# Kernel tuning notes

Hardware: AMD Instinct MI355X
Metric: run time of the kernel (lower is better)

The kernel has to match this reference:

```python
import jax, jax.numpy as jnp
import numpy as np

N_EXPERTS = 6
TOP_K = 2
AUX_COEFF = 0.01
W_SCALE = 0.02  # keep activations in a sane range with random weights


def setup_inputs() -> dict:
    key = jax.random.key(0)
    k1, k2, k3, k4 = jax.random.split(key, 4)
    B, T, D, H = 4, 2048, 1024, 4096
    x = jax.random.normal(k1, (B, T, D), dtype=jnp.float32)
    w_router = jax.random.normal(k2, (D, N_EXPERTS), dtype=jnp.float32) * W_SCALE
    w1 = jax.random.normal(k3, (N_EXPERTS, D, H), dtype=jnp.float32) * W_SCALE
    w2 = jax.random.normal(k4, (N_EXPERTS, H, D), dtype=jnp.float32) * W_SCALE
    return {"x": x, "w_router": w_router, "w1": w1, "w2": w2}


def reference(x, w_router, w1, w2):
    B, T, D = x.shape
    x_flat = x.reshape(-1, D)                              # (N, D)
    router_logits = x_flat @ w_router                      # (N, E)
    router_probs = jax.nn.softmax(router_logits, axis=-1)
    top_probs, top_idx = jax.lax.top_k(router_probs, TOP_K)  # (N, K)
    top_probs = top_probs / jnp.sum(top_probs, axis=-1, keepdims=True)
    # combine weights per (token, expert): sum over k slots hitting expert e
    onehot = jax.nn.one_hot(top_idx, N_EXPERTS, dtype=x.dtype)  # (N, K, E)
    comb = jnp.einsum('nke,nk->ne', onehot, top_probs)          # (N, E)
    out = jnp.zeros_like(x_flat)
    for e in range(N_EXPERTS):
        h = jax.nn.gelu(x_flat @ w1[e], approximate=False)      # (N, H)
        out = out + comb[:, e:e + 1] * (h @ w2[e])              # (N, D)
    tokens_per_expert = jnp.mean(router_probs, axis=0)          # (E,)
    uniform = jnp.full_like(tokens_per_expert, 1.0 / N_EXPERTS)
    aux_loss = AUX_COEFF * jnp.mean((tokens_per_expert - uniform) ** 2)
    return out.reshape(B, T, D), aux_loss
```

## Files before the change

### kernel.cpp

```cpp
#include <hip/hip_runtime.h>

#define N_TOK 8192
#define DDIM  1024
#define HDIM  4096
#define NEXP  6
#define RBLOCKS (N_TOK / 4)
#define SBLOCKS 32

typedef unsigned short ushort_t;
typedef __bf16 bf16_t;
typedef bf16_t bf16x8 __attribute__((ext_vector_type(8)));
typedef float f32x4 __attribute__((ext_vector_type(4)));

typedef const __attribute__((address_space(1))) void* gptr_t;
typedef __attribute__((address_space(3))) void* lptr_t;

__device__ __forceinline__ void g2l16(const void* g, void* l) {
    __builtin_amdgcn_global_load_lds((gptr_t)g, (lptr_t)l, 16, 0, 0);
}

__device__ __forceinline__ ushort_t f2bf(float f) {
    unsigned int u = __float_as_uint(f);
    unsigned int r = (u + 0x7FFFu + ((u >> 16) & 1u)) >> 16;
    return (ushort_t)r;
}

__global__ void transpose_bf16_kernel(const float* __restrict__ src, ushort_t* __restrict__ dst,
                                      int R, int C) {
    __shared__ float tile[32][33];
    size_t msz = (size_t)R * C;
    src += (size_t)blockIdx.z * msz;
    dst += (size_t)blockIdx.z * msz;
    int c0 = blockIdx.x * 32, r0 = blockIdx.y * 32;
    int tx = threadIdx.x & 31, ty = threadIdx.x >> 5;
#pragma unroll
    for (int i = 0; i < 4; ++i)
        tile[ty + 8 * i][tx] = src[(size_t)(r0 + ty + 8 * i) * C + c0 + tx];
    __syncthreads();
#pragma unroll
    for (int i = 0; i < 4; ++i)
        dst[(size_t)(c0 + ty + 8 * i) * R + r0 + tx] = f2bf(tile[tx][ty + 8 * i]);
}

__global__ void router_kernel(const float* __restrict__ x, const float* __restrict__ wr,
                              ushort_t* __restrict__ xb,
                              int* __restrict__ tok_e, float* __restrict__ tok_w,
                              float* __restrict__ part_p, int* __restrict__ part_c) {
    __shared__ float bsum[NEXP];
    __shared__ int bcnt[NEXP];
    int wid = threadIdx.x >> 6, l = threadIdx.x & 63;
    if (threadIdx.x < NEXP) { bsum[threadIdx.x] = 0.f; bcnt[threadIdx.x] = 0; }
    __syncthreads();
    int t = blockIdx.x * 4 + wid;
    const float* xr = x + (size_t)t * DDIM;
    ushort_t* xbr = xb + (size_t)t * DDIM;
    float acc[NEXP] = {0.f, 0.f, 0.f, 0.f, 0.f, 0.f};
#pragma unroll
    for (int c = 0; c < 4; ++c) {
        int k0 = c * 256 + l * 4;
        float4 xv = *(const float4*)(xr + k0);
        union { ushort_t u[4]; uint2 v; } ob;
        ob.u[0] = f2bf(xv.x); ob.u[1] = f2bf(xv.y); ob.u[2] = f2bf(xv.z); ob.u[3] = f2bf(xv.w);
        *(uint2*)(xbr + k0) = ob.v;
        float wv[24];
#pragma unroll
        for (int q = 0; q < 6; ++q)
            *(float4*)(wv + 4 * q) = *(const float4*)(wr + (size_t)k0 * NEXP + 4 * q);
        float xa[4] = {xv.x, xv.y, xv.z, xv.w};
#pragma unroll
        for (int r = 0; r < 4; ++r)
#pragma unroll
            for (int e = 0; e < NEXP; ++e) acc[e] += xa[r] * wv[r * NEXP + e];
    }
#pragma unroll
    for (int e = 0; e < NEXP; ++e)
#pragma unroll
        for (int d = 32; d >= 1; d >>= 1) acc[e] += __shfl_xor(acc[e], d);
    if (l == 0) {
        float m = acc[0];
#pragma unroll
        for (int e = 1; e < NEXP; ++e) m = fmaxf(m, acc[e]);
        float p[NEXP], s = 0.f;
#pragma unroll
        for (int e = 0; e < NEXP; ++e) { p[e] = expf(acc[e] - m); s += p[e]; }
        float inv = 1.0f / s;
#pragma unroll
        for (int e = 0; e < NEXP; ++e) p[e] *= inv;
        int i1 = 0; float b1 = p[0];
#pragma unroll
        for (int e = 1; e < NEXP; ++e) if (p[e] > b1) { b1 = p[e]; i1 = e; }
        int i2 = -1; float b2 = -1.f;
#pragma unroll
        for (int e = 0; e < NEXP; ++e) if (e != i1 && p[e] > b2) { b2 = p[e]; i2 = e; }
        float swn = 1.0f / (b1 + b2);
        tok_e[2 * t] = i1; tok_e[2 * t + 1] = i2;
        tok_w[2 * t] = b1 * swn; tok_w[2 * t + 1] = b2 * swn;
        atomicAdd(&bcnt[i1], 1);
        atomicAdd(&bcnt[i2], 1);
#pragma unroll
        for (int e = 0; e < NEXP; ++e) atomicAdd(&bsum[e], p[e]);
    }
    __syncthreads();
    if (threadIdx.x < NEXP) {
        part_p[(size_t)blockIdx.x * NEXP + threadIdx.x] = bsum[threadIdx.x];
        part_c[(size_t)blockIdx.x * NEXP + threadIdx.x] = bcnt[threadIdx.x];
    }
}

__global__ void finalize_kernel(const float* __restrict__ part_p, const int* __restrict__ part_c,
                                int* __restrict__ counts, int* __restrict__ offs,
                                float* __restrict__ aux_out) {
    __shared__ float redp[NEXP][4];
    __shared__ int redc[NEXP][4];
    int tid = threadIdx.x, wid = tid >> 6, l = tid & 63;
    float myp[NEXP] = {0.f, 0.f, 0.f, 0.f, 0.f, 0.f};
    int myc[NEXP] = {0, 0, 0, 0, 0, 0};
    for (int b = tid; b < RBLOCKS; b += 256) {
#pragma unroll
        for (int e = 0; e < NEXP; ++e) {
            myp[e] += part_p[(size_t)b * NEXP + e];
            myc[e] += part_c[(size_t)b * NEXP + e];
        }
    }
#pragma unroll
    for (int e = 0; e < NEXP; ++e) {
#pragma unroll
        for (int d = 32; d >= 1; d >>= 1) {
            myp[e] += __shfl_xor(myp[e], d);
            myc[e] += __shfl_xor(myc[e], d);
        }
        if (l == 0) { redp[e][wid] = myp[e]; redc[e][wid] = myc[e]; }
    }
    __syncthreads();
    if (tid == 0) {
        int o = 0;
        float s = 0.f;
        for (int e = 0; e < NEXP; ++e) {
            int c = redc[e][0] + redc[e][1] + redc[e][2] + redc[e][3];
            float ps = redp[e][0] + redp[e][1] + redp[e][2] + redp[e][3];
            counts[e] = c;
            offs[e] = o;
            o += c;
            float d = ps / (float)N_TOK - (1.0f / 6.0f);
            s += d * d;
        }
        offs[NEXP] = o;
        aux_out[0] = 0.01f * (s / 6.0f);
    }
}

__global__ void scatter_kernel(const int* __restrict__ tok_e, const float* __restrict__ tok_w,
                               const int* __restrict__ offs, int* __restrict__ cursors,
                               int* __restrict__ slot_token, float* __restrict__ slot_w) {
    __shared__ int lcnt[NEXP], lbase[NEXP];
    int tid = threadIdx.x;
    if (tid < NEXP) lcnt[tid] = 0;
    __syncthreads();
    int t = blockIdx.x * 256 + tid;
    int e0 = tok_e[2 * t], e1 = tok_e[2 * t + 1];
    int r0 = atomicAdd(&lcnt[e0], 1);
    int r1 = atomicAdd(&lcnt[e1], 1);
    __syncthreads();
    if (tid < NEXP) lbase[tid] = atomicAdd(&cursors[tid], lcnt[tid]);
    __syncthreads();
    int i0 = offs[e0] + lbase[e0] + r0;
    slot_token[i0] = t; slot_w[i0] = tok_w[2 * t];
    int i1 = offs[e1] + lbase[e1] + r1;
    slot_token[i1] = t; slot_w[i1] = tok_w[2 * t + 1];
}

template <int LAYER>
__global__ __launch_bounds__(256, 2)
void moe_gemm_kernel(const ushort_t* __restrict__ A, const ushort_t* __restrict__ Bt,
                     ushort_t* __restrict__ Hout, float* __restrict__ Out,
                     const int* __restrict__ slot_token, const float* __restrict__ slot_w,
                     const int* __restrict__ offs, const int* __restrict__ counts) {
    constexpr int Kd = (LAYER == 1) ? DDIM : HDIM;
    constexpr int Nd = (LAYER == 1) ? HDIM : DDIM;
    const int e = blockIdx.z;
    const int cnt = counts[e];
    const int mbase = blockIdx.y * 128;
    if (mbase >= cnt) return;
    const int nbase = blockIdx.x * 256;
    const int off = offs[e];
    const ushort_t* Bte = Bt + (size_t)e * ((size_t)Nd * Kd);

    __shared__ __align__(16) ushort_t sA[128 * 32];
    __shared__ __align__(16) ushort_t sB[256 * 32];

    const int tid = threadIdx.x;
    const int wid = tid >> 6, l = tid & 63;

    size_t aoff[2];
#pragma unroll
    for (int j = 0; j < 2; ++j) {
        int p = j * 256 + tid;
        int row = p >> 2, slot = p & 3;
        int cs = slot ^ ((row >> 1) & 3);
        int gr = mbase + row;
        int grc = gr < cnt - 1 ? gr : cnt - 1;
        size_t arow = (LAYER == 1) ? (size_t)slot_token[off + grc] * DDIM
                                   : (size_t)(off + grc) * HDIM;
        aoff[j] = arow + (size_t)cs * 8;
    }
    size_t boff[4];
#pragma unroll
    for (int j = 0; j < 4; ++j) {
        int p = j * 256 + tid;
        int row = p >> 2, slot = p & 3;
        int cs = slot ^ ((row >> 1) & 3);
        boff[j] = (size_t)(nbase + row) * Kd + (size_t)cs * 8;
    }

    const int lm = l & 15, kg = l >> 4;
    const int wm = (wid & 1) * 64, wn = (wid >> 1) * 128;
    const char* sAb = (const char*)sA;
    const char* sBb = (const char*)sB;
    int aOffs[4], bOffs[8];
#pragma unroll
    for (int fr = 0; fr < 4; ++fr) {
        int ar = wm + fr * 16 + lm;
        aOffs[fr] = ar * 64 + ((kg ^ ((ar >> 1) & 3)) << 4);
    }
#pragma unroll
    for (int fr = 0; fr < 8; ++fr) {
        int br = wn + fr * 16 + lm;
        bOffs[fr] = br * 64 + ((kg ^ ((br >> 1) & 3)) << 4);
    }

    f32x4 acc[4][8] = {};

    for (int kt = 0; kt < Kd; kt += 32) {
        g2l16(A + aoff[0] + kt,   sA + wid * 512);
        g2l16(A + aoff[1] + kt,   sA + 2048 + wid * 512);
        g2l16(Bte + boff[0] + kt, sB + wid * 512);
        g2l16(Bte + boff[1] + kt, sB + 2048 + wid * 512);
        g2l16(Bte + boff[2] + kt, sB + 4096 + wid * 512);
        g2l16(Bte + boff[3] + kt, sB + 6144 + wid * 512);
        __syncthreads();
        bf16x8 af[4], bfv[8];
#pragma unroll
        for (int fr = 0; fr < 4; ++fr) af[fr] = *(const bf16x8*)(sAb + aOffs[fr]);
#pragma unroll
        for (int fr = 0; fr < 8; ++fr) bfv[fr] = *(const bf16x8*)(sBb + bOffs[fr]);
#pragma unroll
        for (int i = 0; i < 4; ++i)
#pragma unroll
            for (int n = 0; n < 8; ++n)
                acc[i][n] = __builtin_amdgcn_mfma_f32_16x16x32_bf16(af[i], bfv[n], acc[i][n], 0, 0, 0);
        __syncthreads();
    }

    if (LAYER == 1) {
#pragma unroll
        for (int i = 0; i < 4; ++i) {
#pragma unroll
            for (int r = 0; r < 4; ++r) {
                int grow = mbase + wm + i * 16 + kg * 4 + r;
                if (grow < cnt) {
                    size_t hbase = (size_t)(off + grow) * HDIM + nbase + wn + lm;
#pragma unroll
                    for (int n = 0; n < 8; ++n) {
                        float v = acc[i][n][r];
                        float u = -1.5957691216f * v * (1.0f + 0.044715f * v * v);
                        float g = v / (1.0f + __expf(u));
                        Hout[hbase + n * 16] = f2bf(g);
                    }
                }
            }
        }
    } else {
#pragma unroll
        for (int i = 0; i < 4; ++i) {
#pragma unroll
            for (int r = 0; r < 4; ++r) {
                int grow = mbase + wm + i * 16 + kg * 4 + r;
                if (grow < cnt) {
                    int si = off + grow;
                    int tok = slot_token[si];
                    float wgt = slot_w[si];
                    float* obase = Out + (size_t)tok * DDIM + nbase + wn + lm;
#pragma unroll
                    for (int n = 0; n < 8; ++n)
                        atomicAdd(obase + n * 16, wgt * acc[i][n][r]);
                }
            }
        }
    }
}

extern "C" void kernel_launch(void* const* d_in, const int* in_sizes, int n_in,
                              void* d_out, int out_size, void* d_ws, size_t ws_size,
                              hipStream_t stream) {
    const float* x  = (const float*)d_in[0];
    const float* wr = (const float*)d_in[1];
    const float* w1 = (const float*)d_in[2];
    const float* w2 = (const float*)d_in[3];
    float* out = (float*)d_out;

    char* ws = (char*)d_ws;
    size_t o = 0;
    ushort_t* xb   = (ushort_t*)(ws + o); o += (size_t)N_TOK * DDIM * 2;
    ushort_t* w1t  = (ushort_t*)(ws + o); o += (size_t)NEXP * HDIM * DDIM * 2;
    ushort_t* w2t  = (ushort_t*)(ws + o); o += (size_t)NEXP * DDIM * HDIM * 2;
    ushort_t* hbuf = (ushort_t*)(ws + o); o += (size_t)2 * N_TOK * HDIM * 2;
    int*   tok_e   = (int*)(ws + o);   o += (size_t)N_TOK * 2 * 4;
    float* tok_w   = (float*)(ws + o); o += (size_t)N_TOK * 2 * 4;
    int*   slot_token = (int*)(ws + o);   o += (size_t)2 * N_TOK * 4;
    float* slot_w     = (float*)(ws + o); o += (size_t)2 * N_TOK * 4;
    float* part_p  = (float*)(ws + o); o += (size_t)RBLOCKS * NEXP * 4;
    int*   part_c  = (int*)(ws + o);   o += (size_t)RBLOCKS * NEXP * 4;
    int*   counts  = (int*)(ws + o);   o += 32;
    int*   cursors = (int*)(ws + o);   o += 32;
    int*   offs    = (int*)(ws + o);   o += 32;

    hipMemsetAsync(d_out, 0, (size_t)out_size * sizeof(float), stream);
    hipMemsetAsync(cursors, 0, 32, stream);

    router_kernel<<<dim3(RBLOCKS), 256, 0, stream>>>(x, wr, xb, tok_e, tok_w, part_p, part_c);
    transpose_bf16_kernel<<<dim3(HDIM / 32, DDIM / 32, NEXP), 256, 0, stream>>>(w1, w1t, DDIM, HDIM);
    transpose_bf16_kernel<<<dim3(DDIM / 32, HDIM / 32, NEXP), 256, 0, stream>>>(w2, w2t, HDIM, DDIM);
    finalize_kernel<<<dim3(1), 256, 0, stream>>>(part_p, part_c, counts, offs, out + (size_t)N_TOK * DDIM);
    scatter_kernel<<<dim3(SBLOCKS), 256, 0, stream>>>(tok_e, tok_w, offs, cursors, slot_token, slot_w);
    moe_gemm_kernel<1><<<dim3(HDIM / 256, N_TOK / 128, NEXP), 256, 0, stream>>>(
        xb, w1t, hbuf, nullptr, slot_token, slot_w, offs, counts);
    moe_gemm_kernel<2><<<dim3(DDIM / 256, N_TOK / 128, NEXP), 256, 0, stream>>>(
        hbuf, w2t, nullptr, out, slot_token, slot_w, offs, counts);
}
```

Baseline: 560.5 us.

## Triple-buffer MoE GEMM shared-memory tiles with async global-to-LDS prefetch

Replaces the single-buffered K loop in the expert GEMM kernels with a three-stage LDS ring. Two tiles are prefetched ahead via global_load_lds, and a vmcnt wait plus one barrier per iteration replace the two syncthreads. The aim is to overlap global loads with MFMA work instead of stalling on every tile. LDS use rises to 72KB per block through dynamic shared memory, which may limit occupancy relative to the launch bound of 2 blocks per CU.

Result: faster. 486.5 us, median of 3 (-13.2%).

```diff
diff --git a/kernel.cpp b/kernel.cpp
--- a/kernel.cpp
+++ b/kernel.cpp
@@ -169,6 +169,18 @@
     slot_token[i1] = t; slot_w[i1] = tok_w[2 * t + 1];
 }
 
+
+#define STAGE(BI, KTE) do { \
+    ushort_t* bA_ = sbase + (BI) * 12288; \
+    ushort_t* bB_ = bA_ + 4096; \
+    g2l16(A + aoff[0] + (KTE),   bA_ + wid * 512); \
+    g2l16(A + aoff[1] + (KTE),   bA_ + 2048 + wid * 512); \
+    g2l16(Bte + boff[0] + (KTE), bB_ + wid * 512); \
+    g2l16(Bte + boff[1] + (KTE), bB_ + 2048 + wid * 512); \
+    g2l16(Bte + boff[2] + (KTE), bB_ + 4096 + wid * 512); \
+    g2l16(Bte + boff[3] + (KTE), bB_ + 6144 + wid * 512); \
+  } while (0)
+
 template <int LAYER>
 __global__ __launch_bounds__(256, 2)
 void moe_gemm_kernel(const ushort_t* __restrict__ A, const ushort_t* __restrict__ Bt,
@@ -177,6 +189,10 @@
                      const int* __restrict__ offs, const int* __restrict__ counts) {
     constexpr int Kd = (LAYER == 1) ? DDIM : HDIM;
     constexpr int Nd = (LAYER == 1) ? HDIM : DDIM;
+    constexpr int NT = Kd / 32;
+    extern __shared__ __align__(16) char smem[];
+    ushort_t* sbase = (ushort_t*)smem;
+
     const int e = blockIdx.z;
     const int cnt = counts[e];
     const int mbase = blockIdx.y * 128;
@@ -184,9 +200,6 @@
     const int nbase = blockIdx.x * 256;
     const int off = offs[e];
     const ushort_t* Bte = Bt + (size_t)e * ((size_t)Nd * Kd);
-
-    __shared__ __align__(16) ushort_t sA[128 * 32];
-    __shared__ __align__(16) ushort_t sB[256 * 32];
 
     const int tid = threadIdx.x;
     const int wid = tid >> 6, l = tid & 63;
@@ -214,8 +227,6 @@
 
     const int lm = l & 15, kg = l >> 4;
     const int wm = (wid & 1) * 64, wn = (wid >> 1) * 128;
-    const char* sAb = (const char*)sA;
-    const char* sBb = (const char*)sB;
     int aOffs[4], bOffs[8];
 #pragma unroll
     for (int fr = 0; fr < 4; ++fr) {
@@ -230,25 +241,35 @@
 
     f32x4 acc[4][8] = {};
 
-    for (int kt = 0; kt < Kd; kt += 32) {
-        g2l16(A + aoff[0] + kt,   sA + wid * 512);
-        g2l16(A + aoff[1] + kt,   sA + 2048 + wid * 512);
-        g2l16(Bte + boff[0] + kt, sB + wid * 512);
-        g2l16(Bte + boff[1] + kt, sB + 2048 + wid * 512);
-        g2l16(Bte + boff[2] + kt, sB + 4096 + wid * 512);
-        g2l16(Bte + boff[3] + kt, sB + 6144 + wid * 512);
-        __syncthreads();
+    STAGE(0, 0);
+    STAGE(1, 32);
+    asm volatile("s_waitcnt vmcnt(6)" ::: "memory");
+    __builtin_amdgcn_sched_barrier(0);
+    __builtin_amdgcn_s_barrier();
+
+    int rb = 0;
+    for (int t = 0; t < NT; ++t) {
+        int sb = rb + 2; if (sb >= 3) sb -= 3;
+        if (t + 2 < NT) STAGE(sb, (t + 2) * 32);
+        const char* bA = (const char*)(sbase + rb * 12288);
+        const char* bB = bA + 8192;
         bf16x8 af[4], bfv[8];
 #pragma unroll
-        for (int fr = 0; fr < 4; ++fr) af[fr] = *(const bf16x8*)(sAb + aOffs[fr]);
-#pragma unroll
-        for (int fr = 0; fr < 8; ++fr) bfv[fr] = *(const bf16x8*)(sBb + bOffs[fr]);
+        for (int fr = 0; fr < 4; ++fr) af[fr] = *(const bf16x8*)(bA + aOffs[fr]);
+#pragma unroll
+        for (int fr = 0; fr < 8; ++fr) bfv[fr] = *(const bf16x8*)(bB + bOffs[fr]);
 #pragma unroll
         for (int i = 0; i < 4; ++i)
 #pragma unroll
             for (int n = 0; n < 8; ++n)
                 acc[i][n] = __builtin_amdgcn_mfma_f32_16x16x32_bf16(af[i], bfv[n], acc[i][n], 0, 0, 0);
-        __syncthreads();
+        if (t < NT - 1) {
+            if (t + 3 <= NT) { asm volatile("s_waitcnt vmcnt(6)" ::: "memory"); }
+            else             { asm volatile("s_waitcnt vmcnt(0)" ::: "memory"); }
+            __builtin_amdgcn_sched_barrier(0);
+            __builtin_amdgcn_s_barrier();
+        }
+        rb = rb + 1; if (rb >= 3) rb -= 3;
     }
 
     if (LAYER == 1) {
@@ -288,6 +309,7 @@
         }
     }
 }
+#undef STAGE
 
 extern "C" void kernel_launch(void* const* d_in, const int* in_sizes, int n_in,
                               void* d_out, int out_size, void* d_ws, size_t ws_size,
@@ -317,13 +339,16 @@
     hipMemsetAsync(d_out, 0, (size_t)out_size * sizeof(float), stream);
     hipMemsetAsync(cursors, 0, 32, stream);
 
+    hipFuncSetAttribute((const void*)moe_gemm_kernel<1>, hipFuncAttributeMaxDynamicSharedMemorySize, 73728);
+    hipFuncSetAttribute((const void*)moe_gemm_kernel<2>, hipFuncAttributeMaxDynamicSharedMemorySize, 73728);
+
     router_kernel<<<dim3(RBLOCKS), 256, 0, stream>>>(x, wr, xb, tok_e, tok_w, part_p, part_c);
     transpose_bf16_kernel<<<dim3(HDIM / 32, DDIM / 32, NEXP), 256, 0, stream>>>(w1, w1t, DDIM, HDIM);
     transpose_bf16_kernel<<<dim3(DDIM / 32, HDIM / 32, NEXP), 256, 0, stream>>>(w2, w2t, HDIM, DDIM);
     finalize_kernel<<<dim3(1), 256, 0, stream>>>(part_p, part_c, counts, offs, out + (size_t)N_TOK * DDIM);
     scatter_kernel<<<dim3(SBLOCKS), 256, 0, stream>>>(tok_e, tok_w, offs, cursors, slot_token, slot_w);
-    moe_gemm_kernel<1><<<dim3(HDIM / 256, N_TOK / 128, NEXP), 256, 0, stream>>>(
+    moe_gemm_kernel<1><<<dim3(HDIM / 256, N_TOK / 128, NEXP), 256, 73728, stream>>>(
         xb, w1t, hbuf, nullptr, slot_token, slot_w, offs, counts);
-    moe_gemm_kernel<2><<<dim3(DDIM / 256, N_TOK / 128, NEXP), 256, 0, stream>>>(
+    moe_gemm_kernel<2><<<dim3(DDIM / 256, N_TOK / 128, NEXP), 256, 73728, stream>>>(
         hbuf, w2t, nullptr, out, slot_token, slot_w, offs, counts);
 }
```
